# Kernel tuning notes

Measured on AMD Instinct MI355X. Metric: run time of the kernel, lower is better.

The kernel has to match this reference:

```python
import jax, jax.numpy as jnp
import numpy as np

L, H, C, V, T_BLK = 12, 12, 768, 50257, 1024
D = C // H  # head dim = 64


def _layernorm(x, g, b, eps=1e-5):
    m = jnp.mean(x, axis=-1, keepdims=True)
    v = jnp.mean(jnp.square(x - m), axis=-1, keepdims=True)
    return (x - m) * jax.lax.rsqrt(v + eps) * g + b


def setup_inputs() -> dict:
    key = jax.random.key(0)
    ks = jax.random.split(key, 8)
    B, T = 8, 1024
    s = 0.02
    sp = 0.02 / np.sqrt(2 * L)  # c_proj special init
    return {
        "idx": jax.random.randint(ks[0], (B, T), 0, V, dtype=jnp.int32),
        "wte": jax.random.normal(ks[1], (V, C), jnp.float32) * s,
        "wpe": jax.random.normal(ks[2], (T_BLK, C), jnp.float32) * s,
        "ln1_g": jnp.ones((L, C), jnp.float32),
        "ln1_b": jnp.zeros((L, C), jnp.float32),
        "w_qkv": jax.random.normal(ks[3], (L, C, 3 * C), jnp.float32) * s,
        "b_qkv": jnp.zeros((L, 3 * C), jnp.float32),
        "w_ao": jax.random.normal(ks[4], (L, C, C), jnp.float32) * sp,
        "b_ao": jnp.zeros((L, C), jnp.float32),
        "ln2_g": jnp.ones((L, C), jnp.float32),
        "ln2_b": jnp.zeros((L, C), jnp.float32),
        "w_fc": jax.random.normal(ks[5], (L, C, 4 * C), jnp.float32) * s,
        "b_fc": jnp.zeros((L, 4 * C), jnp.float32),
        "w_mo": jax.random.normal(ks[6], (L, 4 * C, C), jnp.float32) * sp,
        "b_mo": jnp.zeros((L, C), jnp.float32),
        "lnf_g": jnp.ones((C,), jnp.float32),
        "lnf_b": jnp.zeros((C,), jnp.float32),
    }


def reference(idx, wte, wpe, ln1_g, ln1_b, w_qkv, b_qkv, w_ao, b_ao,
              ln2_g, ln2_b, w_fc, b_fc, w_mo, b_mo, lnf_g, lnf_b):
    B, T = idx.shape
    scale = 1.0 / np.sqrt(D)
    causal = jnp.tril(jnp.ones((T, T), dtype=bool))  # [T,T]

    x = wte[idx] + wpe[:T]  # [B,T,C]

    def block(x, p):
        g1, b1, wq, bq, wo, bo, g2, b2_, wf, bf, w2, b2m = p
        h = _layernorm(x, g1, b1)
        qkv = h @ wq + bq  # [B,T,3C]
        q, k, v = jnp.split(qkv, 3, axis=-1)
        q = q.reshape(B, T, H, D)
        k = k.reshape(B, T, H, D)
        v = v.reshape(B, T, H, D)
        att = jnp.einsum('bqhd,bkhd->bhqk', q, k) * scale
        att = jnp.where(causal, att, -jnp.inf)
        att = jax.nn.softmax(att, axis=-1)
        y = jnp.einsum('bhqk,bkhd->bqhd', att, v).reshape(B, T, C)
        x = x + y @ wo + bo
        h2 = _layernorm(x, g2, b2_)
        x = x + jax.nn.gelu(h2 @ wf + bf, approximate=False) @ w2 + b2m
        return x, None

    params = (ln1_g, ln1_b, w_qkv, b_qkv, w_ao, b_ao,
              ln2_g, ln2_b, w_fc, b_fc, w_mo, b_mo)
    x, _ = jax.lax.scan(block, x, params)

    x = _layernorm(x, lnf_g, lnf_b)
    # inference path: logits only for last position, lm_head tied to wte
    logits = x[:, -1:, :] @ wte.T  # [B,1,V]
    return logits
```

## Files before the change

### kernel.cpp

```cpp
#include <hip/hip_runtime.h>

#define B_ 8
#define T_ 1024
#define C_ 768
#define H_ 12
#define L_ 12
#define V_ 50257

typedef __bf16 bf16_t;
typedef __bf16 bf16x8 __attribute__((ext_vector_type(8)));
typedef __bf16 bf16x4 __attribute__((ext_vector_type(4)));
typedef float f32x4 __attribute__((ext_vector_type(4)));

#define AS1 __attribute__((address_space(1)))
#define AS3 __attribute__((address_space(3)))

__device__ __forceinline__ unsigned short f2bf(float f) {
  bf16_t h = (bf16_t)f;
  return __builtin_bit_cast(unsigned short, h);
}

__device__ __forceinline__ unsigned short bfbits(bf16_t h) {
  return __builtin_bit_cast(unsigned short, h);
}

__device__ __forceinline__ float fast_gelu(float v) {
  const float xe = v * 0.70710678118f;
  const float ax = fabsf(xe);
  const float t = 1.0f / fmaf(0.3275911f, ax, 1.0f);
  float poly = fmaf(t, 1.061405429f, -1.453152027f);
  poly = fmaf(t, poly, 1.421413741f);
  poly = fmaf(t, poly, -0.284496736f);
  poly = fmaf(t, poly, 0.254829592f);
  poly *= t;
  float er = 1.0f - poly * __expf(-ax * ax);
  er = (xe < 0.0f) ? -er : er;
  return 0.5f * v * (1.0f + er);
}

__global__ __launch_bounds__(192) void embed_kernel(
    const int* __restrict__ idx, const float* __restrict__ wte,
    const float* __restrict__ wpe, float* __restrict__ xf)
{
  const int bt = blockIdx.x;
  const int t = bt & (T_ - 1);
  const int tok = idx[bt];
  const int c4 = threadIdx.x << 2;
  float4 a = *(const float4*)(wte + (size_t)tok * C_ + c4);
  float4 p = *(const float4*)(wpe + (size_t)t * C_ + c4);
  float4 r; r.x = a.x + p.x; r.y = a.y + p.y; r.z = a.z + p.z; r.w = a.w + p.w;
  *(float4*)(xf + (size_t)bt * C_ + c4) = r;
}

template<bool LAST>
__global__ __launch_bounds__(256) void ln_kernel(
    const float* __restrict__ x, const float* __restrict__ gw,
    const float* __restrict__ bw, unsigned short* __restrict__ obf,
    float* __restrict__ of)
{
  __shared__ float red[8];
  const size_t row = LAST ? ((size_t)blockIdx.x * T_ + (T_ - 1)) : (size_t)blockIdx.x;
  const float* xr = x + row * C_;
  const int t = threadIdx.x;
  float v0 = xr[t], v1 = xr[t + 256], v2 = xr[t + 512];
  float s = v0 + v1 + v2;
  #pragma unroll
  for (int off = 32; off; off >>= 1) s += __shfl_xor(s, off);
  if ((t & 63) == 0) red[t >> 6] = s;
  __syncthreads();
  const float mean = (red[0] + red[1] + red[2] + red[3]) * (1.0f / C_);
  const float d0 = v0 - mean, d1 = v1 - mean, d2 = v2 - mean;
  float ss = d0 * d0 + d1 * d1 + d2 * d2;
  #pragma unroll
  for (int off = 32; off; off >>= 1) ss += __shfl_xor(ss, off);
  if ((t & 63) == 0) red[4 + (t >> 6)] = ss;
  __syncthreads();
  const float var = (red[4] + red[5] + red[6] + red[7]) * (1.0f / C_);
  const float rs = rsqrtf(var + 1e-5f);
  float o0 = d0 * rs * gw[t] + bw[t];
  float o1 = d1 * rs * gw[t + 256] + bw[t + 256];
  float o2 = d2 * rs * gw[t + 512] + bw[t + 512];
  if (LAST) {
    float* orow = of + (size_t)blockIdx.x * C_;
    orow[t] = o0; orow[t + 256] = o1; orow[t + 512] = o2;
  } else {
    unsigned short* orow = obf + row * C_;
    orow[t] = f2bf(o0); orow[t + 256] = f2bf(o1); orow[t + 512] = f2bf(o2);
  }
}

__global__ __launch_bounds__(256) void cvtw4_kernel(
    const float* __restrict__ wq, const float* __restrict__ wa,
    const float* __restrict__ wf, const float* __restrict__ wm,
    unsigned short* __restrict__ out)
{
  __shared__ float tile[32][33];
  const int i = blockIdx.x;
  const float* W; unsigned short* Wt; int K, N, tix;
  if (i < 1728)      { W = wq; Wt = out;                 K = C_;     N = 3 * C_; tix = i; }
  else if (i < 2304) { W = wa; Wt = out + 3 * C_ * C_;   K = C_;     N = C_;     tix = i - 1728; }
  else if (i < 4608) { W = wf; Wt = out + 4 * C_ * C_;   K = C_;     N = 4 * C_; tix = i - 2304; }
  else               { W = wm; Wt = out + 8 * C_ * C_;   K = 4 * C_; N = C_;     tix = i - 4608; }
  const int ntx = N >> 5;
  const int kb = (tix / ntx) << 5, nb = (tix % ntx) << 5;
  const int t = threadIdx.x;
  {
    const int k = t >> 3, n4 = (t & 7) << 2;
    float4 v = *(const float4*)(W + (size_t)(kb + k) * N + nb + n4);
    tile[k][n4] = v.x; tile[k][n4 + 1] = v.y; tile[k][n4 + 2] = v.z; tile[k][n4 + 3] = v.w;
  }
  __syncthreads();
  {
    const int n = t >> 3, k4 = (t & 7) << 2;
    ushort4 o;
    o.x = f2bf(tile[k4][n]);     o.y = f2bf(tile[k4 + 1][n]);
    o.z = f2bf(tile[k4 + 2][n]); o.w = f2bf(tile[k4 + 3][n]);
    *(ushort4*)(Wt + (size_t)(nb + n) * K + kb + k4) = o;
  }
}

template<int EPI>
__global__ __launch_bounds__(256, 2) void gemm_bt(
    const unsigned short* __restrict__ A, const unsigned short* __restrict__ Bt,
    const float* __restrict__ bias, float* __restrict__ Cf,
    unsigned short* __restrict__ Cb, int M, int N, int K, int nx)
{
  (void)M; (void)nx;
  __shared__ unsigned short As[2][128 * 64];
  __shared__ unsigned short Bs[2][128 * 64];
  const int tid = threadIdx.x;
  const int lane = tid & 63;
  const int w = tid >> 6;
  const int wr = w >> 1, wc = w & 1;
  const int l15 = lane & 15, l4 = lane >> 4;
  const int swz = lane & 7;

  const int bid = blockIdx.x;
  const int xcd = bid & 7;
  const int j = bid >> 3;
  const int mblk = xcd * 8 + (j & 7);
  const int nblk = j >> 3;
  const int m0 = mblk * 128, n0 = nblk * 128;

  f32x4 acc[4][4] = {};

  const int srow = lane >> 3;
  const int schunk = (lane & 7) ^ srow;
  const unsigned short* aSrc = A + (size_t)(m0 + w * 32 + srow) * K + schunk * 8;
  const unsigned short* bSrc = Bt + (size_t)(n0 + w * 32 + srow) * K + schunk * 8;
  const int ldsRowBase = (w * 32) * 64;

  auto stage = [&](int kt, int p) {
    const int k0 = kt << 6;
    #pragma unroll
    for (int jj = 0; jj < 4; ++jj)
      __builtin_amdgcn_global_load_lds(
          (const AS1 unsigned int*)(aSrc + (size_t)jj * 8 * K + k0),
          (AS3 unsigned int*)(&As[p][ldsRowBase + jj * 8 * 64]), 16, 0, 0);
    #pragma unroll
    for (int jj = 0; jj < 4; ++jj)
      __builtin_amdgcn_global_load_lds(
          (const AS1 unsigned int*)(bSrc + (size_t)jj * 8 * K + k0),
          (AS3 unsigned int*)(&Bs[p][ldsRowBase + jj * 8 * 64]), 16, 0, 0);
  };

  auto compute = [&](int p) {
    const unsigned short* aw = &As[p][(wr * 64) * 64];
    const unsigned short* bw2 = &Bs[p][(wc * 64) * 64];
    #pragma unroll
    for (int ks = 0; ks < 2; ++ks) {
      bf16x8 af[4], bf[4];
      #pragma unroll
      for (int mf = 0; mf < 4; ++mf)
        af[mf] = *(const bf16x8*)(aw + (mf * 16 + l15) * 64 + (((ks << 2) | l4) ^ swz) * 8);
      #pragma unroll
      for (int nf = 0; nf < 4; ++nf)
        bf[nf] = *(const bf16x8*)(bw2 + (nf * 16 + l15) * 64 + (((ks << 2) | l4) ^ swz) * 8);
      __builtin_amdgcn_s_setprio(1);
      #pragma unroll
      for (int mf = 0; mf < 4; ++mf)
        #pragma unroll
        for (int nf = 0; nf < 4; ++nf)
          acc[mf][nf] = __builtin_amdgcn_mfma_f32_16x16x32_bf16(af[mf], bf[nf], acc[mf][nf], 0, 0, 0);
      __builtin_amdgcn_s_setprio(0);
    }
  };

  const int nk = K >> 6;
  stage(0, 0);
  for (int kt = 0; kt < nk - 1; ++kt) {
    const int p = kt & 1;
    stage(kt + 1, p ^ 1);
    asm volatile("s_waitcnt vmcnt(8)" ::: "memory");
    __builtin_amdgcn_s_barrier();
    compute(p);
    __builtin_amdgcn_s_barrier();
  }
  asm volatile("s_waitcnt vmcnt(0)" ::: "memory");
  __builtin_amdgcn_s_barrier();
  compute((nk - 1) & 1);

  #pragma unroll
  for (int mf = 0; mf < 4; ++mf) {
    #pragma unroll
    for (int nf = 0; nf < 4; ++nf) {
      const int col = n0 + wc * 64 + nf * 16 + l15;
      const float bv = bias[col];
      int hh = 0, dd = 0;
      unsigned short* qkvo = nullptr;
      if constexpr (EPI == 3) {
        const int which = col / C_;
        const int rem = col - which * C_;
        hh = rem >> 6; dd = rem & 63;
        qkvo = Cb + (size_t)which * ((size_t)B_ * H_ * T_ * 64);
      }
      #pragma unroll
      for (int i = 0; i < 4; ++i) {
        const int row = m0 + wr * 64 + mf * 16 + l4 * 4 + i;
        float v = acc[mf][nf][i] + bv;
        if constexpr (EPI == 1) {
          Cf[(size_t)row * N + col] += v;
        } else if constexpr (EPI == 2) {
          Cb[(size_t)row * N + col] = f2bf(fast_gelu(v));
        } else {
          const int bb = row >> 10, tt = row & (T_ - 1);
          qkvo[(((size_t)bb * H_ + hh) * T_ + tt) * 64 + dd] = f2bf(v);
        }
      }
    }
  }
}

__global__ __launch_bounds__(256) void attn_kernel(
    const unsigned short* __restrict__ Qb, const unsigned short* __restrict__ Kb,
    const unsigned short* __restrict__ Vb, unsigned short* __restrict__ y)
{
  const int pb = blockIdx.x / 96;
  const int bh = blockIdx.x % 96;
  const int h = bh % H_;
  const int b = bh / H_;
  const int tid = threadIdx.x, lane = tid & 63, w = tid >> 6;
  const int l15 = lane & 15, l4 = lane >> 4;

  const int qband0 = pb * 64 + w * 16;
  const int qband1 = (15 - pb) * 64 + w * 16;
  const int NT = (17 - pb) >> 1;

  __shared__ unsigned short Ks[128 * 64];
  __shared__ unsigned short Vt[64 * 136];
  __shared__ unsigned short Pb[4][32 * 74];

  bf16x8 qf[2][2];
  {
    const unsigned short* q0p = Qb + ((size_t)bh * T_ + qband0) * 64;
    const unsigned short* q1p = Qb + ((size_t)bh * T_ + qband1) * 64;
    #pragma unroll
    for (int ks = 0; ks < 2; ++ks) {
      qf[0][ks] = *(const bf16x8*)(q0p + l15 * 64 + ks * 32 + l4 * 8);
      qf[1][ks] = *(const bf16x8*)(q1p + l15 * 64 + ks * 32 + l4 * 8);
    }
    #pragma unroll
    for (int mf = 0; mf < 2; ++mf)
      #pragma unroll
      for (int ks = 0; ks < 2; ++ks)
        #pragma unroll
        for (int jj = 0; jj < 8; ++jj)
          qf[mf][ks][jj] = (bf16_t)((float)qf[mf][ks][jj] * 0.125f);
  }

  bf16x8 ones;
  #pragma unroll
  for (int jj = 0; jj < 8; ++jj) ones[jj] = (bf16_t)1.0f;

  f32x4 o[2][4] = {};
  f32x4 rs[2] = {};

  const unsigned short* kb0 = Kb + (size_t)bh * T_ * 64;
  const unsigned short* vb0 = Vb + (size_t)bh * T_ * 64;
  const int ck = w;
  const int skey = lane;
  const int sw = (skey & 7);

  bf16x8 kr0, kr1, kr2, kr3, vr0, vr1, vr2, vr3;
  {
    const unsigned short* kp = kb0 + (size_t)skey * 64;
    const unsigned short* vp = vb0 + (size_t)skey * 64;
    kr0 = *(const bf16x8*)(kp + ck * 8);
    kr1 = *(const bf16x8*)(kp + (ck + 4) * 8);
    kr2 = *(const bf16x8*)(kp + 64 * 64 + ck * 8);
    kr3 = *(const bf16x8*)(kp + 64 * 64 + (ck + 4) * 8);
    vr0 = *(const bf16x8*)(vp + ck * 8);
    vr1 = *(const bf16x8*)(vp + (ck + 4) * 8);
    vr2 = *(const bf16x8*)(vp + 64 * 64 + ck * 8);
    vr3 = *(const bf16x8*)(vp + 64 * 64 + (ck + 4) * 8);
  }

  for (int kt = 0; kt < NT; ++kt) {
    const int k0 = kt << 7;
    __syncthreads();
    *(bf16x8*)(Ks + skey * 64 + ((ck ^ sw) * 8)) = kr0;
    *(bf16x8*)(Ks + skey * 64 + (((ck + 4) ^ sw) * 8)) = kr1;
    *(bf16x8*)(Ks + (skey + 64) * 64 + ((ck ^ sw) * 8)) = kr2;
    *(bf16x8*)(Ks + (skey + 64) * 64 + (((ck + 4) ^ sw) * 8)) = kr3;
    #pragma unroll
    for (int jj = 0; jj < 8; ++jj) {
      Vt[(ck * 8 + jj) * 136 + skey]            = bfbits(vr0[jj]);
      Vt[((ck + 4) * 8 + jj) * 136 + skey]      = bfbits(vr1[jj]);
      Vt[(ck * 8 + jj) * 136 + skey + 64]       = bfbits(vr2[jj]);
      Vt[((ck + 4) * 8 + jj) * 136 + skey + 64] = bfbits(vr3[jj]);
    }
    __syncthreads();
    if (kt + 1 < NT) {
      const int kn = (kt + 1) << 7;
      const unsigned short* kp = kb0 + (size_t)(kn + skey) * 64;
      const unsigned short* vp = vb0 + (size_t)(kn + skey) * 64;
      kr0 = *(const bf16x8*)(kp + ck * 8);
      kr1 = *(const bf16x8*)(kp + (ck + 4) * 8);
      kr2 = *(const bf16x8*)(kp + 64 * 64 + ck * 8);
      kr3 = *(const bf16x8*)(kp + 64 * 64 + (ck + 4) * 8);
      vr0 = *(const bf16x8*)(vp + ck * 8);
      vr1 = *(const bf16x8*)(vp + (ck + 4) * 8);
      vr2 = *(const bf16x8*)(vp + 64 * 64 + ck * 8);
      vr3 = *(const bf16x8*)(vp + 64 * 64 + (ck + 4) * 8);
    }

    #pragma unroll
    for (int h2 = 0; h2 < 2; ++h2) {
      const int kh0 = k0 + h2 * 64;
      const bool act0 = (kh0 <= qband0 + 15);
      const bool act1 = (kh0 <= qband1 + 15);
      if (!act0 && !act1) continue;

      f32x4 s[2][4] = {};
      __builtin_amdgcn_s_setprio(1);
      #pragma unroll
      for (int ks = 0; ks < 2; ++ks) {
        #pragma unroll
        for (int nfk = 0; nfk < 4; ++nfk) {
          const int key = h2 * 64 + nfk * 16 + l15;
          bf16x8 kf = *(const bf16x8*)(Ks + key * 64 + ((((ks << 2) | l4) ^ (l15 & 7)) * 8));
          if (act0) s[0][nfk] = __builtin_amdgcn_mfma_f32_16x16x32_bf16(qf[0][ks], kf, s[0][nfk], 0, 0, 0);
          if (act1) s[1][nfk] = __builtin_amdgcn_mfma_f32_16x16x32_bf16(qf[1][ks], kf, s[1][nfk], 0, 0, 0);
        }
      }
      __builtin_amdgcn_s_setprio(0);

      #pragma unroll
      for (int mf = 0; mf < 2; ++mf) {
        const bool act = mf ? act1 : act0;
        if (!act) continue;
        const int qb0 = mf ? qband1 : qband0;
        const int qrow = qb0 + l4 * 4;
        const bool fullt = (kh0 + 63) <= qb0;
        float pvv[4][4];
        #pragma unroll
        for (int i = 0; i < 4; ++i) {
          const int q = qrow + i;
          #pragma unroll
          for (int nfk = 0; nfk < 4; ++nfk) {
            const bool on = fullt || (kh0 + nfk * 16 + l15 <= q);
            pvv[nfk][i] = on ? __expf(s[mf][nfk][i]) : 0.0f;
          }
        }
        #pragma unroll
        for (int nfk = 0; nfk < 4; ++nfk)
          #pragma unroll
          for (int i = 0; i < 4; ++i)
            Pb[w][(mf * 16 + l4 * 4 + i) * 74 + nfk * 16 + l15] = f2bf(pvv[nfk][i]);
      }

      bf16x8 pa[2][2];
      #pragma unroll
      for (int mf = 0; mf < 2; ++mf)
        if (mf ? act1 : act0)
          #pragma unroll
          for (int k2 = 0; k2 < 2; ++k2)
            pa[mf][k2] = *(const bf16x8*)(Pb[w] + (mf * 16 + l15) * 74 + k2 * 32 + l4 * 8);
      __builtin_amdgcn_s_setprio(1);
      #pragma unroll
      for (int nf = 0; nf < 4; ++nf) {
        const int d = nf * 16 + l15;
        #pragma unroll
        for (int k2 = 0; k2 < 2; ++k2) {
          bf16x8 vf = *(const bf16x8*)(Vt + d * 136 + h2 * 64 + k2 * 32 + l4 * 8);
          if (act0) o[0][nf] = __builtin_amdgcn_mfma_f32_16x16x32_bf16(pa[0][k2], vf, o[0][nf], 0, 0, 0);
          if (act1) o[1][nf] = __builtin_amdgcn_mfma_f32_16x16x32_bf16(pa[1][k2], vf, o[1][nf], 0, 0, 0);
        }
      }
      #pragma unroll
      for (int k2 = 0; k2 < 2; ++k2) {
        if (act0) rs[0] = __builtin_amdgcn_mfma_f32_16x16x32_bf16(pa[0][k2], ones, rs[0], 0, 0, 0);
        if (act1) rs[1] = __builtin_amdgcn_mfma_f32_16x16x32_bf16(pa[1][k2], ones, rs[1], 0, 0, 0);
      }
      __builtin_amdgcn_s_setprio(0);
    }
  }

  #pragma unroll
  for (int mf = 0; mf < 2; ++mf) {
    const int qb0 = mf ? qband1 : qband0;
    #pragma unroll
    for (int i = 0; i < 4; ++i) {
      const float inv = 1.0f / rs[mf][i];
      const int q = qb0 + l4 * 4 + i;
      unsigned short* yr = y + (size_t)(b * T_ + q) * C_ + h * 64;
      #pragma unroll
      for (int nf = 0; nf < 4; ++nf)
        yr[nf * 16 + l15] = f2bf(o[mf][nf][i] * inv);
    }
  }
}

__global__ __launch_bounds__(256) void head_kernel(
    const float* __restrict__ lnf, const float* __restrict__ wte,
    float* __restrict__ out)
{
  __shared__ float xs[B_ * C_];
  for (int i = threadIdx.x; i < B_ * C_; i += 256) xs[i] = lnf[i];
  __syncthreads();
  const int w = threadIdx.x >> 6, lane = threadIdx.x & 63;
  const int v = blockIdx.x * 4 + w;
  if (v >= V_) return;
  const float* wv = wte + (size_t)v * C_ + lane * 12;
  float4 w0 = *(const float4*)(wv);
  float4 w1 = *(const float4*)(wv + 4);
  float4 w2 = *(const float4*)(wv + 8);
  float acc[B_];
  #pragma unroll
  for (int bb = 0; bb < B_; ++bb) {
    const float* xr = xs + bb * C_ + lane * 12;
    float4 x0 = *(const float4*)(xr);
    float4 x1 = *(const float4*)(xr + 4);
    float4 x2 = *(const float4*)(xr + 8);
    acc[bb] = w0.x * x0.x + w0.y * x0.y + w0.z * x0.z + w0.w * x0.w
            + w1.x * x1.x + w1.y * x1.y + w1.z * x1.z + w1.w * x1.w
            + w2.x * x2.x + w2.y * x2.y + w2.z * x2.z + w2.w * x2.w;
  }
  #pragma unroll
  for (int off = 32; off; off >>= 1) {
    #pragma unroll
    for (int bb = 0; bb < B_; ++bb)
      acc[bb] += __shfl_xor(acc[bb], off);
  }
  if (lane == 0) {
    #pragma unroll
    for (int bb = 0; bb < B_; ++bb)
      out[(size_t)bb * V_ + v] = acc[bb];
  }
}

extern "C" void kernel_launch(void* const* d_in, const int* in_sizes, int n_in,
                              void* d_out, int out_size, void* d_ws, size_t ws_size,
                              hipStream_t stream)
{
  (void)in_sizes; (void)n_in; (void)out_size; (void)ws_size;
  const int*   idx   = (const int*)d_in[0];
  const float* wte   = (const float*)d_in[1];
  const float* wpe   = (const float*)d_in[2];
  const float* ln1_g = (const float*)d_in[3];
  const float* ln1_b = (const float*)d_in[4];
  const float* w_qkv = (const float*)d_in[5];
  const float* b_qkv = (const float*)d_in[6];
  const float* w_ao  = (const float*)d_in[7];
  const float* b_ao  = (const float*)d_in[8];
  const float* ln2_g = (const float*)d_in[9];
  const float* ln2_b = (const float*)d_in[10];
  const float* w_fc  = (const float*)d_in[11];
  const float* b_fc  = (const float*)d_in[12];
  const float* w_mo  = (const float*)d_in[13];
  const float* b_mo  = (const float*)d_in[14];
  const float* lnf_g = (const float*)d_in[15];
  const float* lnf_b = (const float*)d_in[16];

  char* ws = (char*)d_ws;
  size_t off = 0;
  auto wsalloc = [&](size_t bytes) -> void* {
    void* p = ws + off;
    off += (bytes + 255) & ~(size_t)255;
    return p;
  };
  const size_t SZH = (size_t)B_ * H_ * T_ * 64;
  float* xf             = (float*)wsalloc((size_t)B_ * T_ * C_ * 4);
  unsigned short* qkv3  = (unsigned short*)wsalloc(3 * SZH * 2);
  unsigned short* a_in  = (unsigned short*)wsalloc((size_t)B_ * T_ * C_ * 2);
  unsigned short* act2  = (unsigned short*)wsalloc((size_t)B_ * T_ * 4 * C_ * 2);
  unsigned short* wbuf  = (unsigned short*)wsalloc((size_t)12 * C_ * C_ * 2);
  float* lnfb           = (float*)wsalloc((size_t)B_ * C_ * 4);

  const size_t OFF_AO = (size_t)3 * C_ * C_;
  const size_t OFF_FC = (size_t)4 * C_ * C_;
  const size_t OFF_MO = (size_t)8 * C_ * C_;
  const int MROWS = B_ * T_;

  embed_kernel<<<B_ * T_, 192, 0, stream>>>(idx, wte, wpe, xf);

  for (int l = 0; l < L_; ++l) {
    ln_kernel<false><<<B_ * T_, 256, 0, stream>>>(xf, ln1_g + l * C_, ln1_b + l * C_, a_in, nullptr);
    cvtw4_kernel<<<6912, 256, 0, stream>>>(
        w_qkv + (size_t)l * C_ * 3 * C_, w_ao + (size_t)l * C_ * C_,
        w_fc + (size_t)l * C_ * 4 * C_, w_mo + (size_t)l * 4 * C_ * C_, wbuf);
    gemm_bt<3><<<64 * 18, 256, 0, stream>>>(a_in, wbuf, b_qkv + l * 3 * C_, nullptr, qkv3, MROWS, 3 * C_, C_, 18);
    attn_kernel<<<8 * B_ * H_, 256, 0, stream>>>(qkv3, qkv3 + SZH, qkv3 + 2 * SZH, a_in);
    gemm_bt<1><<<64 * 6, 256, 0, stream>>>(a_in, wbuf + OFF_AO, b_ao + l * C_, xf, nullptr, MROWS, C_, C_, 6);
    ln_kernel<false><<<B_ * T_, 256, 0, stream>>>(xf, ln2_g + l * C_, ln2_b + l * C_, a_in, nullptr);
    gemm_bt<2><<<64 * 24, 256, 0, stream>>>(a_in, wbuf + OFF_FC, b_fc + l * 4 * C_, nullptr, act2, MROWS, 4 * C_, C_, 24);
    gemm_bt<1><<<64 * 6, 256, 0, stream>>>(act2, wbuf + OFF_MO, b_mo + l * C_, xf, nullptr, MROWS, C_, 4 * C_, 6);
  }

  ln_kernel<true><<<B_, 256, 0, stream>>>(xf, lnf_g, lnf_b, nullptr, lnfb);
  head_kernel<<<(V_ + 3) / 4, 256, 0, stream>>>(lnfb, wte, (float*)d_out);
}
```

Baseline: 3.527 ms.

## Use 256x128 single-buffered GEMM tiles for QKV and FC projections

Adds a gemm_w kernel with 256x128 output tiles (each wave computes 128x64), used for the QKV and FC GEMMs. The larger tile gives more B-tile reuse and more MFMA work per LDS fetch. In exchange it drops LDS double-buffering, so each K-step is load, sync, compute, sync with no load/compute overlap. It also halves the grid size, which may reduce occupancy and the number of workgroups per CU.

```diff
diff --git a/kernel.cpp b/kernel.cpp
--- a/kernel.cpp
+++ b/kernel.cpp
@@ -120,14 +120,14 @@
 }
 
 template<int EPI>
-__global__ __launch_bounds__(256, 2) void gemm_bt(
+__global__ __launch_bounds__(256, 2) void gemm_w(
     const unsigned short* __restrict__ A, const unsigned short* __restrict__ Bt,
-    const float* __restrict__ bias, float* __restrict__ Cf,
-    unsigned short* __restrict__ Cb, int M, int N, int K, int nx)
-{
-  (void)M; (void)nx;
-  __shared__ unsigned short As[2][128 * 64];
-  __shared__ unsigned short Bs[2][128 * 64];
+    const float* __restrict__ bias, unsigned short* __restrict__ Cb,
+    int N, int K, int nx)
+{
+  (void)nx;
+  __shared__ unsigned short As[256 * 64];
+  __shared__ unsigned short Bs[128 * 64];
   const int tid = threadIdx.x;
   const int lane = tid & 63;
   const int w = tid >> 6;
@@ -138,70 +138,68 @@
   const int bid = blockIdx.x;
   const int xcd = bid & 7;
   const int j = bid >> 3;
-  const int mblk = xcd * 8 + (j & 7);
-  const int nblk = j >> 3;
-  const int m0 = mblk * 128, n0 = nblk * 128;
-
-  f32x4 acc[4][4] = {};
+  const int mblk = xcd * 4 + (j & 3);
+  const int nblk = j >> 2;
+  const int m0 = mblk * 256, n0 = nblk * 128;
+
+  f32x4 acc[8][4] = {};
 
   const int srow = lane >> 3;
   const int schunk = (lane & 7) ^ srow;
-  const unsigned short* aSrc = A + (size_t)(m0 + w * 32 + srow) * K + schunk * 8;
+  const unsigned short* aSrc = A + (size_t)(m0 + w * 64 + srow) * K + schunk * 8;
   const unsigned short* bSrc = Bt + (size_t)(n0 + w * 32 + srow) * K + schunk * 8;
-  const int ldsRowBase = (w * 32) * 64;
-
-  auto stage = [&](int kt, int p) {
+
+  auto stage = [&](int kt) {
     const int k0 = kt << 6;
     #pragma unroll
-    for (int jj = 0; jj < 4; ++jj)
+    for (int jj = 0; jj < 8; ++jj)
       __builtin_amdgcn_global_load_lds(
           (const AS1 unsigned int*)(aSrc + (size_t)jj * 8 * K + k0),
-          (AS3 unsigned int*)(&As[p][ldsRowBase + jj * 8 * 64]), 16, 0, 0);
+          (AS3 unsigned int*)(&As[(w * 64 + jj * 8) * 64]), 16, 0, 0);
     #pragma unroll
     for (int jj = 0; jj < 4; ++jj)
       __builtin_amdgcn_global_load_lds(
           (const AS1 unsigned int*)(bSrc + (size_t)jj * 8 * K + k0),
-          (AS3 unsigned int*)(&Bs[p][ldsRowBase + jj * 8 * 64]), 16, 0, 0);
+          (AS3 unsigned int*)(&Bs[(w * 32 + jj * 8) * 64]), 16, 0, 0);
   };
 
-  auto compute = [&](int p) {
-    const unsigned short* aw = &As[p][(wr * 64) * 64];
-    const unsigned short* bw2 = &Bs[p][(wc * 64) * 64];
+  auto compute = [&]() {
+    const unsigned short* aw = &As[(wr * 128) * 64];
+    const unsigned short* bw2 = &Bs[(wc * 64) * 64];
     #pragma unroll
     for (int ks = 0; ks < 2; ++ks) {
-      bf16x8 af[4], bf[4];
-      #pragma unroll
-      for (int mf = 0; mf < 4; ++mf)
-        af[mf] = *(const bf16x8*)(aw + (mf * 16 + l15) * 64 + (((ks << 2) | l4) ^ swz) * 8);
+      const int co = (((ks << 2) | l4) ^ swz) * 8;
+      bf16x8 bf[4];
       #pragma unroll
       for (int nf = 0; nf < 4; ++nf)
-        bf[nf] = *(const bf16x8*)(bw2 + (nf * 16 + l15) * 64 + (((ks << 2) | l4) ^ swz) * 8);
-      __builtin_amdgcn_s_setprio(1);
-      #pragma unroll
-      for (int mf = 0; mf < 4; ++mf)
-        #pragma unroll
-        for (int nf = 0; nf < 4; ++nf)
-          acc[mf][nf] = __builtin_amdgcn_mfma_f32_16x16x32_bf16(af[mf], bf[nf], acc[mf][nf], 0, 0, 0);
-      __builtin_amdgcn_s_setprio(0);
+        bf[nf] = *(const bf16x8*)(bw2 + (nf * 16 + l15) * 64 + co);
+      #pragma unroll
+      for (int fh = 0; fh < 2; ++fh) {
+        bf16x8 af[4];
+        #pragma unroll
+        for (int f = 0; f < 4; ++f)
+          af[f] = *(const bf16x8*)(aw + ((fh * 4 + f) * 16 + l15) * 64 + co);
+        __builtin_amdgcn_s_setprio(1);
+        #pragma unroll
+        for (int f = 0; f < 4; ++f)
+          #pragma unroll
+          for (int nf = 0; nf < 4; ++nf)
+            acc[fh * 4 + f][nf] = __builtin_amdgcn_mfma_f32_16x16x32_bf16(af[f], bf[nf], acc[fh * 4 + f][nf], 0, 0, 0);
+        __builtin_amdgcn_s_setprio(0);
+      }
     }
   };
 
   const int nk = K >> 6;
-  stage(0, 0);
-  for (int kt = 0; kt < nk - 1; ++kt) {
-    const int p = kt & 1;
-    stage(kt + 1, p ^ 1);
-    asm volatile("s_waitcnt vmcnt(8)" ::: "memory");
-    __builtin_amdgcn_s_barrier();
-    compute(p);
-    __builtin_amdgcn_s_barrier();
-  }
-  asm volatile("s_waitcnt vmcnt(0)" ::: "memory");
-  __builtin_amdgcn_s_barrier();
-  compute((nk - 1) & 1);
-
-  #pragma unroll
-  for (int mf = 0; mf < 4; ++mf) {
+  for (int kt = 0; kt < nk; ++kt) {
+    stage(kt);
+    __syncthreads();
+    compute();
+    __syncthreads();
+  }
+
+  #pragma unroll
+  for (int f = 0; f < 8; ++f) {
     #pragma unroll
     for (int nf = 0; nf < 4; ++nf) {
       const int col = n0 + wc * 64 + nf * 16 + l15;
@@ -216,15 +214,114 @@
       }
       #pragma unroll
       for (int i = 0; i < 4; ++i) {
+        const int row = m0 + wr * 128 + f * 16 + l4 * 4 + i;
+        float v = acc[f][nf][i] + bv;
+        if constexpr (EPI == 2) {
+          Cb[(size_t)row * N + col] = f2bf(fast_gelu(v));
+        } else {
+          const int bb = row >> 10, tt = row & (T_ - 1);
+          qkvo[(((size_t)bb * H_ + hh) * T_ + tt) * 64 + dd] = f2bf(v);
+        }
+      }
+    }
+  }
+}
+
+template<int EPI>
+__global__ __launch_bounds__(256, 2) void gemm_bt(
+    const unsigned short* __restrict__ A, const unsigned short* __restrict__ Bt,
+    const float* __restrict__ bias, float* __restrict__ Cf,
+    unsigned short* __restrict__ Cb, int M, int N, int K, int nx)
+{
+  (void)M; (void)nx;
+  __shared__ unsigned short As[2][128 * 64];
+  __shared__ unsigned short Bs[2][128 * 64];
+  const int tid = threadIdx.x;
+  const int lane = tid & 63;
+  const int w = tid >> 6;
+  const int wr = w >> 1, wc = w & 1;
+  const int l15 = lane & 15, l4 = lane >> 4;
+  const int swz = lane & 7;
+
+  const int bid = blockIdx.x;
+  const int xcd = bid & 7;
+  const int j = bid >> 3;
+  const int mblk = xcd * 8 + (j & 7);
+  const int nblk = j >> 3;
+  const int m0 = mblk * 128, n0 = nblk * 128;
+
+  f32x4 acc[4][4] = {};
+
+  const int srow = lane >> 3;
+  const int schunk = (lane & 7) ^ srow;
+  const unsigned short* aSrc = A + (size_t)(m0 + w * 32 + srow) * K + schunk * 8;
+  const unsigned short* bSrc = Bt + (size_t)(n0 + w * 32 + srow) * K + schunk * 8;
+  const int ldsRowBase = (w * 32) * 64;
+
+  auto stage = [&](int kt, int p) {
+    const int k0 = kt << 6;
+    #pragma unroll
+    for (int jj = 0; jj < 4; ++jj)
+      __builtin_amdgcn_global_load_lds(
+          (const AS1 unsigned int*)(aSrc + (size_t)jj * 8 * K + k0),
+          (AS3 unsigned int*)(&As[p][ldsRowBase + jj * 8 * 64]), 16, 0, 0);
+    #pragma unroll
+    for (int jj = 0; jj < 4; ++jj)
+      __builtin_amdgcn_global_load_lds(
+          (const AS1 unsigned int*)(bSrc + (size_t)jj * 8 * K + k0),
+          (AS3 unsigned int*)(&Bs[p][ldsRowBase + jj * 8 * 64]), 16, 0, 0);
+  };
+
+  auto compute = [&](int p) {
+    const unsigned short* aw = &As[p][(wr * 64) * 64];
+    const unsigned short* bw2 = &Bs[p][(wc * 64) * 64];
+    #pragma unroll
+    for (int ks = 0; ks < 2; ++ks) {
+      bf16x8 af[4], bf[4];
+      #pragma unroll
+      for (int mf = 0; mf < 4; ++mf)
+        af[mf] = *(const bf16x8*)(aw + (mf * 16 + l15) * 64 + (((ks << 2) | l4) ^ swz) * 8);
+      #pragma unroll
+      for (int nf = 0; nf < 4; ++nf)
+        bf[nf] = *(const bf16x8*)(bw2 + (nf * 16 + l15) * 64 + (((ks << 2) | l4) ^ swz) * 8);
+      __builtin_amdgcn_s_setprio(1);
+      #pragma unroll
+      for (int mf = 0; mf < 4; ++mf)
+        #pragma unroll
+        for (int nf = 0; nf < 4; ++nf)
+          acc[mf][nf] = __builtin_amdgcn_mfma_f32_16x16x32_bf16(af[mf], bf[nf], acc[mf][nf], 0, 0, 0);
+      __builtin_amdgcn_s_setprio(0);
+    }
+  };
+
+  const int nk = K >> 6;
+  stage(0, 0);
+  for (int kt = 0; kt < nk - 1; ++kt) {
+    const int p = kt & 1;
+    stage(kt + 1, p ^ 1);
+    asm volatile("s_waitcnt vmcnt(8)" ::: "memory");
+    __builtin_amdgcn_s_barrier();
+    compute(p);
+    __builtin_amdgcn_s_barrier();
+  }
+  asm volatile("s_waitcnt vmcnt(0)" ::: "memory");
+  __builtin_amdgcn_s_barrier();
+  compute((nk - 1) & 1);
+
+  #pragma unroll
+  for (int mf = 0; mf < 4; ++mf) {
+    #pragma unroll
+    for (int nf = 0; nf < 4; ++nf) {
+      const int col = n0 + wc * 64 + nf * 16 + l15;
+      const float bv = bias[col];
+      #pragma unroll
+      for (int i = 0; i < 4; ++i) {
         const int row = m0 + wr * 64 + mf * 16 + l4 * 4 + i;
         float v = acc[mf][nf][i] + bv;
         if constexpr (EPI == 1) {
           Cf[(size_t)row * N + col] += v;
         } else if constexpr (EPI == 2) {
           Cb[(size_t)row * N + col] = f2bf(fast_gelu(v));
-        } else {
-          const int bb = row >> 10, tt = row & (T_ - 1);
-          qkvo[(((size_t)bb * H_ + hh) * T_ + tt) * 64 + dd] = f2bf(v);
         }
       }
     }
@@ -499,11 +596,11 @@
     cvtw4_kernel<<<6912, 256, 0, stream>>>(
         w_qkv + (size_t)l * C_ * 3 * C_, w_ao + (size_t)l * C_ * C_,
         w_fc + (size_t)l * C_ * 4 * C_, w_mo + (size_t)l * 4 * C_ * C_, wbuf);
-    gemm_bt<3><<<64 * 18, 256, 0, stream>>>(a_in, wbuf, b_qkv + l * 3 * C_, nullptr, qkv3, MROWS, 3 * C_, C_, 18);
+    gemm_w<3><<<32 * 18, 256, 0, stream>>>(a_in, wbuf, b_qkv + l * 3 * C_, qkv3, 3 * C_, C_, 18);
     attn_kernel<<<8 * B_ * H_, 256, 0, stream>>>(qkv3, qkv3 + SZH, qkv3 + 2 * SZH, a_in);
     gemm_bt<1><<<64 * 6, 256, 0, stream>>>(a_in, wbuf + OFF_AO, b_ao + l * C_, xf, nullptr, MROWS, C_, C_, 6);
     ln_kernel<false><<<B_ * T_, 256, 0, stream>>>(xf, ln2_g + l * C_, ln2_b + l * C_, a_in, nullptr);
-    gemm_bt<2><<<64 * 24, 256, 0, stream>>>(a_in, wbuf + OFF_FC, b_fc + l * 4 * C_, nullptr, act2, MROWS, 4 * C_, C_, 24);
+    gemm_w<2><<<32 * 24, 256, 0, stream>>>(a_in, wbuf + OFF_FC, b_fc + l * 4 * C_, act2, 4 * C_, C_, 24);
     gemm_bt<1><<<64 * 6, 256, 0, stream>>>(act2, wbuf + OFF_MO, b_mo + l * C_, xf, nullptr, MROWS, C_, 4 * C_, 6);
   }
 
```

Measured after the change: 3.571 ms. Within noise of the previous version (+1.2%).

## Write V transposed in QKV epilogue and read V fragments directly from global

Applied to the files above, without the earlier changes.

The QKV GEMM epilogue now stores V in a [b,h,d,t] transposed layout instead of [b,h,t,d]. The attention kernel drops the shared-memory V transpose buffer and its scalar transposing stores, and loads V fragments for the PV MFMA straight from global/L2 memory. This removes LDS transpose work and shared memory use, but puts uncached global loads inside the inner loop with no prefetch. It also makes the epilogue's V stores strided along t, which are poorly coalesced.

```diff
diff --git a/kernel.cpp b/kernel.cpp
--- a/kernel.cpp
+++ b/kernel.cpp
@@ -206,10 +206,10 @@
     for (int nf = 0; nf < 4; ++nf) {
       const int col = n0 + wc * 64 + nf * 16 + l15;
       const float bv = bias[col];
-      int hh = 0, dd = 0;
+      int which = 0, hh = 0, dd = 0;
       unsigned short* qkvo = nullptr;
       if constexpr (EPI == 3) {
-        const int which = col / C_;
+        which = col / C_;
         const int rem = col - which * C_;
         hh = rem >> 6; dd = rem & 63;
         qkvo = Cb + (size_t)which * ((size_t)B_ * H_ * T_ * 64);
@@ -224,7 +224,10 @@
           Cb[(size_t)row * N + col] = f2bf(fast_gelu(v));
         } else {
           const int bb = row >> 10, tt = row & (T_ - 1);
-          qkvo[(((size_t)bb * H_ + hh) * T_ + tt) * 64 + dd] = f2bf(v);
+          if (which == 2)
+            qkvo[(((size_t)bb * H_ + hh) * 64 + dd) * T_ + tt] = f2bf(v);
+          else
+            qkvo[(((size_t)bb * H_ + hh) * T_ + tt) * 64 + dd] = f2bf(v);
         }
       }
     }
@@ -247,7 +250,6 @@
   const int NT = (17 - pb) >> 1;
 
   __shared__ unsigned short Ks[128 * 64];
-  __shared__ unsigned short Vt[64 * 136];
   __shared__ unsigned short Pb[4][32 * 74];
 
   bf16x8 qf[2][2];
@@ -276,23 +278,18 @@
   f32x4 rs[2] = {};
 
   const unsigned short* kb0 = Kb + (size_t)bh * T_ * 64;
-  const unsigned short* vb0 = Vb + (size_t)bh * T_ * 64;
+  const unsigned short* vb0 = Vb + (size_t)bh * 64 * T_;
   const int ck = w;
   const int skey = lane;
   const int sw = (skey & 7);
 
-  bf16x8 kr0, kr1, kr2, kr3, vr0, vr1, vr2, vr3;
+  bf16x8 kr0, kr1, kr2, kr3;
   {
     const unsigned short* kp = kb0 + (size_t)skey * 64;
-    const unsigned short* vp = vb0 + (size_t)skey * 64;
     kr0 = *(const bf16x8*)(kp + ck * 8);
     kr1 = *(const bf16x8*)(kp + (ck + 4) * 8);
     kr2 = *(const bf16x8*)(kp + 64 * 64 + ck * 8);
     kr3 = *(const bf16x8*)(kp + 64 * 64 + (ck + 4) * 8);
-    vr0 = *(const bf16x8*)(vp + ck * 8);
-    vr1 = *(const bf16x8*)(vp + (ck + 4) * 8);
-    vr2 = *(const bf16x8*)(vp + 64 * 64 + ck * 8);
-    vr3 = *(const bf16x8*)(vp + 64 * 64 + (ck + 4) * 8);
   }
 
   for (int kt = 0; kt < NT; ++kt) {
@@ -302,26 +299,14 @@
     *(bf16x8*)(Ks + skey * 64 + (((ck + 4) ^ sw) * 8)) = kr1;
     *(bf16x8*)(Ks + (skey + 64) * 64 + ((ck ^ sw) * 8)) = kr2;
     *(bf16x8*)(Ks + (skey + 64) * 64 + (((ck + 4) ^ sw) * 8)) = kr3;
-    #pragma unroll
-    for (int jj = 0; jj < 8; ++jj) {
-      Vt[(ck * 8 + jj) * 136 + skey]            = bfbits(vr0[jj]);
-      Vt[((ck + 4) * 8 + jj) * 136 + skey]      = bfbits(vr1[jj]);
-      Vt[(ck * 8 + jj) * 136 + skey + 64]       = bfbits(vr2[jj]);
-      Vt[((ck + 4) * 8 + jj) * 136 + skey + 64] = bfbits(vr3[jj]);
-    }
     __syncthreads();
     if (kt + 1 < NT) {
       const int kn = (kt + 1) << 7;
       const unsigned short* kp = kb0 + (size_t)(kn + skey) * 64;
-      const unsigned short* vp = vb0 + (size_t)(kn + skey) * 64;
       kr0 = *(const bf16x8*)(kp + ck * 8);
       kr1 = *(const bf16x8*)(kp + (ck + 4) * 8);
       kr2 = *(const bf16x8*)(kp + 64 * 64 + ck * 8);
       kr3 = *(const bf16x8*)(kp + 64 * 64 + (ck + 4) * 8);
-      vr0 = *(const bf16x8*)(vp + ck * 8);
-      vr1 = *(const bf16x8*)(vp + (ck + 4) * 8);
-      vr2 = *(const bf16x8*)(vp + 64 * 64 + ck * 8);
-      vr3 = *(const bf16x8*)(vp + 64 * 64 + (ck + 4) * 8);
     }
 
     #pragma unroll
@@ -380,9 +365,10 @@
       #pragma unroll
       for (int nf = 0; nf < 4; ++nf) {
         const int d = nf * 16 + l15;
+        const unsigned short* vrow = vb0 + (size_t)d * T_ + kh0;
         #pragma unroll
         for (int k2 = 0; k2 < 2; ++k2) {
-          bf16x8 vf = *(const bf16x8*)(Vt + d * 136 + h2 * 64 + k2 * 32 + l4 * 8);
+          bf16x8 vf = *(const bf16x8*)(vrow + k2 * 32 + l4 * 8);
           if (act0) o[0][nf] = __builtin_amdgcn_mfma_f32_16x16x32_bf16(pa[0][k2], vf, o[0][nf], 0, 0, 0);
           if (act1) o[1][nf] = __builtin_amdgcn_mfma_f32_16x16x32_bf16(pa[1][k2], vf, o[1][nf], 0, 0, 0);
         }
```

Result: slower. 3.952 ms (+12.0%).
